# Kernel optimization log

Hardware: AMD Instinct MI355X
Metric: run time of the kernel (lower is better)

Reference implementation:

```python
import jax, jax.numpy as jnp
import numpy as np
import math

N_EMBD = 1024
N_HEAD = 16
BLOCK = 2048
SPARSITY = 0.25
B, T = 2, 2048


def _make_mask_logits(rng):
    # Replicates the patterned init in SparseMixtureAttention.__init__.
    S = BLOCK
    logits = np.empty((N_HEAD, S, S), dtype=np.float32)
    for h in range(N_HEAD):
        if h % 3 == 0:  # banded pattern (bandwidth 16)
            i = np.arange(S)
            band = (np.abs(i[:, None] - i[None, :]) <= 16)
            logits[h] = np.where(band, rng.standard_normal((S, S)) + 2.0,
                                 rng.standard_normal((S, S)) - 2.0)
        elif h % 3 == 1:  # strided pattern: every 4th column
            strided = (np.arange(S)[None, :] % 4 == 0)
            logits[h] = np.where(strided, rng.standard_normal((S, S)) + 2.0,
                                 rng.standard_normal((S, S)) - 2.0)
        else:  # random pattern with given sparsity
            rnd = rng.random((S, S)) < SPARSITY
            logits[h] = np.where(rnd, rng.standard_normal((S, S)) + 2.0,
                                 rng.standard_normal((S, S)) - 2.0)
    # keep the diagonal unmasked so no causal row is fully masked (avoids NaN rows)
    d = np.arange(S)
    logits[:, d, d] = np.abs(logits[:, d, d]) + 2.0
    return logits.astype(np.float32)


def setup_inputs() -> dict:
    key = jax.random.key(0)
    ks = jax.random.split(key, 5)
    rng = np.random.default_rng(0)
    return {
        "x": jax.random.normal(ks[0], (B, T, N_EMBD), dtype=jnp.float32),
        "mask_logits": jnp.asarray(_make_mask_logits(rng)),
        "W_attn": jax.random.normal(ks[1], (3 * N_EMBD, N_EMBD), dtype=jnp.float32) * 0.02,
        "b_attn": jnp.zeros((3 * N_EMBD,), dtype=jnp.float32),
        "W_proj": jax.random.normal(ks[2], (N_EMBD, N_EMBD), dtype=jnp.float32) * 0.02,
        "b_proj": jnp.zeros((N_EMBD,), dtype=jnp.float32),
    }


def reference(x, mask_logits, W_attn, b_attn, W_proj, b_proj):
    Bx, Tx, C = x.shape
    H = mask_logits.shape[0]
    D = C // H
    qkv = x @ W_attn.T + b_attn                       # [B,T,3C]
    q, k, v = jnp.split(qkv, 3, axis=-1)
    q = q.reshape(Bx, Tx, H, D)
    k = k.reshape(Bx, Tx, H, D)
    v = v.reshape(Bx, Tx, H, D)
    att = jnp.einsum('bthd,bshd->bhts', q, k) * (1.0 / math.sqrt(D))  # [B,H,T,T]
    # forward value of the STE mask equals the hard mask (probs - probs.detach() == 0)
    keep = jax.nn.sigmoid(mask_logits[:, :Tx, :Tx]) > 0.5             # [H,T,T]
    causal = jnp.tril(jnp.ones((Tx, Tx), dtype=bool))
    mask = causal[None, :, :] & keep                                  # [H,T,T]
    att = jnp.where(mask[None], att, -jnp.inf)
    att = jax.nn.softmax(att, axis=-1)
    y = jnp.einsum('bhts,bshd->bthd', att, v).reshape(Bx, Tx, C)
    return y @ W_proj.T + b_proj
```

## Files before the change

### kernel.cpp

```cpp
#include <hip/hip_runtime.h>
#include <hip/hip_bf16.h>
#include <stdint.h>

typedef unsigned short u16;
typedef unsigned int u32;
typedef unsigned long long u64;
typedef __attribute__((ext_vector_type(8))) short bf16x8;
typedef __attribute__((ext_vector_type(4))) float f32x4;

#define NB 2
#define NH 16
#define TT 2048
#define DD 64
#define CC 1024

__device__ __forceinline__ u16 bf16bits(float f) {
    __hip_bfloat16 h = __float2bfloat16(f);
    return __builtin_bit_cast(unsigned short, h);
}

__device__ __forceinline__ void gload_lds16(const void* g, void* l) {
    __builtin_amdgcn_global_load_lds(
        (const __attribute__((address_space(1))) void*)g,
        (__attribute__((address_space(3))) void*)l, 16, 0, 0);
}

__global__ __launch_bounds__(256) void prep_all(
    const float* __restrict__ x, const float* __restrict__ Wa_f,
    const float* __restrict__ Wp_f, const float* __restrict__ ml,
    u16* __restrict__ xb, u16* __restrict__ wab, u16* __restrict__ wpb,
    unsigned char* __restrict__ mb) {
    const int bid = blockIdx.x;
    if (bid < 512) {
        int idx = bid * 256 + threadIdx.x;
        for (int i = idx; i < 2097152; i += 512 * 256) {
            const float* src; u16* dst; int off;
            if (i < 1048576)      { src = x;    dst = xb;  off = i; }
            else if (i < 1835008) { src = Wa_f; dst = wab; off = i - 1048576; }
            else                  { src = Wp_f; dst = wpb; off = i - 1835008; }
            float4 v = reinterpret_cast<const float4*>(src)[off];
            ushort4 o;
            o.x = bf16bits(v.x); o.y = bf16bits(v.y);
            o.z = bf16bits(v.z); o.w = bf16bits(v.w);
            reinterpret_cast<ushort4*>(dst)[off] = o;
        }
    } else {
        const int wid = ((bid - 512) << 2) + (threadIdx.x >> 6);
        const int lane = threadIdx.x & 63;
        const int i0 = wid & 2047;
        const int hbase = (wid >> 11) << 3;
#pragma unroll 1
        for (int k = 0; k < 8; ++k) {
            int h = hbase + k;
            int i = (k & 1) ? (2047 - i0) : i0;
            int row = h * 2048 + i;
            const float* src = ml + (size_t)row * TT;
            unsigned char* dst = mb + (size_t)row * (TT / 8);
            for (int c8 = lane; c8 * 8 <= i; c8 += 64) {
                const float4* p = reinterpret_cast<const float4*>(src + c8 * 8);
                float4 a = p[0];
                float4 b = p[1];
                unsigned v = 0;
                v |= (a.x > 0.f) ? 1u : 0u;
                v |= (a.y > 0.f) ? 2u : 0u;
                v |= (a.z > 0.f) ? 4u : 0u;
                v |= (a.w > 0.f) ? 8u : 0u;
                v |= (b.x > 0.f) ? 16u : 0u;
                v |= (b.y > 0.f) ? 32u : 0u;
                v |= (b.z > 0.f) ? 64u : 0u;
                v |= (b.w > 0.f) ? 128u : 0u;
                dst[c8] = (unsigned char)v;
            }
        }
    }
}

template <int MODE>
__global__ __launch_bounds__(256) void gemm_bt(
    const u16* __restrict__ A, const u16* __restrict__ Bw,
    const float* __restrict__ bias,
    u16* __restrict__ Qb, u16* __restrict__ Kb, u16* __restrict__ Vtb,
    float* __restrict__ Cout, int Kdim) {
    const int bm = blockIdx.y * 128;
    const int bn = blockIdx.x * 128;
    const int tid = threadIdx.x;
    const int w = tid >> 6, lane = tid & 63;
    const int lrow = lane & 15, lgrp = lane >> 4;
    const int wr = (w >> 1) * 64, wc = (w & 1) * 64;

    __shared__ __align__(16) u16 ABs[2][128 * 64];
    u16* As = ABs[0];
    u16* Bs = ABs[1];

    f32x4 acc[4][4] = {};

    const int nkt = Kdim >> 6;
    for (int kt = 0; kt < nkt; ++kt) {
        const int k0 = kt << 6;
#pragma unroll
        for (int i = 0; i < 4; ++i) {
            int e = i * 2048 + tid * 8;
            int r = e >> 6, c = e & 63;
            gload_lds16(A + (size_t)(bm + r) * Kdim + k0 + c, (char*)As + i * 4096 + w * 1024);
            gload_lds16(Bw + (size_t)(bn + r) * Kdim + k0 + c, (char*)Bs + i * 4096 + w * 1024);
        }
        __syncthreads();
#pragma unroll
        for (int kk = 0; kk < 2; ++kk) {
            bf16x8 af[4], bfz[4];
#pragma unroll
            for (int i = 0; i < 4; ++i)
                af[i] = *reinterpret_cast<const bf16x8*>(&As[(wr + i * 16 + lrow) * 64 + kk * 32 + lgrp * 8]);
#pragma unroll
            for (int i = 0; i < 4; ++i)
                bfz[i] = *reinterpret_cast<const bf16x8*>(&Bs[(wc + i * 16 + lrow) * 64 + kk * 32 + lgrp * 8]);
#pragma unroll
            for (int mi = 0; mi < 4; ++mi)
#pragma unroll
                for (int ni = 0; ni < 4; ++ni)
                    acc[mi][ni] = __builtin_amdgcn_mfma_f32_16x16x32_bf16(af[mi], bfz[ni], acc[mi][ni], 0, 0, 0);
        }
        __syncthreads();
    }

    const int sec = (MODE == 0) ? (bn >> 10) : 1;

    if (MODE == 0 && sec == 2) {
        u16* Tl = &ABs[0][0];
#pragma unroll
        for (int ni = 0; ni < 4; ++ni) {
            int nl = wc + ni * 16 + lrow;
            float bv = bias[bn + nl];
#pragma unroll
            for (int mi = 0; mi < 4; ++mi) {
                int ml2 = wr + mi * 16 + lgrp * 4;
                u64 pk = 0;
#pragma unroll
                for (int j = 0; j < 4; ++j)
                    pk |= (u64)bf16bits(acc[mi][ni][j] + bv) << (16 * j);
                int byte = nl * 256 + ((ml2 * 2) ^ ((nl & 7) << 4));
                *reinterpret_cast<u64*>((char*)Tl + byte) = pk;
            }
        }
        __syncthreads();
        int r = tid >> 1, half = tid & 1;
        int h = ((bn & 1023) >> 6) + (r >> 6);
        int d = r & 63;
        int b = bm >> 11;
        u16* gdst = Vtb + (((size_t)b * NH + h) * DD + d) * TT + (bm & 2047) + half * 64;
#pragma unroll
        for (int c = 0; c < 8; ++c) {
            uint4 v = *reinterpret_cast<const uint4*>(
                (char*)Tl + r * 256 + ((half * 128 + c * 16) ^ ((r & 7) << 4)));
            *reinterpret_cast<uint4*>(gdst + c * 8) = v;
        }
        return;
    }

#pragma unroll
    for (int ni = 0; ni < 4; ++ni) {
        int n = bn + wc + ni * 16 + lrow;
        float bv = bias[n];
#pragma unroll
        for (int mi = 0; mi < 4; ++mi) {
#pragma unroll
            for (int j = 0; j < 4; ++j) {
                int m = bm + wr + mi * 16 + lgrp * 4 + j;
                float v = acc[mi][ni][j] + bv;
                if (MODE == 1) {
                    Cout[(size_t)m * 1024 + n] = v;
                } else {
                    int h = (n & 1023) >> 6;
                    int d = n & 63;
                    int b = m >> 11;
                    int t = m & 2047;
                    if (sec == 0) {
                        Qb[(((size_t)b * NH + h) * TT + t) * DD + d] =
                            bf16bits(v * (0.125f * 1.4426950408889634f));
                    } else {
                        Kb[(((size_t)b * NH + h) * TT + t) * DD + d] = bf16bits(v);
                    }
                }
            }
        }
    }
}

__global__ __launch_bounds__(256) void attn_kernel(
    const u16* __restrict__ Qb, const u16* __restrict__ Kb,
    const u16* __restrict__ Vtb, const unsigned char* __restrict__ mb,
    u16* __restrict__ att_out) {
    const int slot = blockIdx.x >> 4;
    const int h = blockIdx.x & 15;
    const int b = blockIdx.y;
    const int qt = (slot < 16) ? (31 - slot) : (slot - 16);
    const int tid = threadIdx.x;
    const int w = tid >> 6, lane = tid & 63;
    const int lrow = lane & 15, g = lane >> 4;

    __shared__ __align__(16) u16 Ks[2][64 * 64];
    __shared__ __align__(16) u16 Vts[2][64 * 64];
    __shared__ __align__(16) u16 Ps[4][16 * 64];

    const u16* kg_base = &Kb[((size_t)b * NH + h) * TT * DD];
    const u16* vg_base = &Vtb[((size_t)b * NH + h) * DD * TT];

    auto STAGE = [&](int bufi, int kt) {
#pragma unroll
        for (int i = 0; i < 2; ++i) {
            int e = i * 2048 + tid * 8;
            int r = e >> 6, c = e & 63;
            int cs = c ^ ((r & 7) << 3);
            gload_lds16(kg_base + (size_t)kt * 64 * DD + r * DD + cs,
                        (char*)Ks[bufi] + i * 4096 + w * 1024);
            gload_lds16(vg_base + kt * 64 + (size_t)r * TT + cs,
                        (char*)Vts[bufi] + i * 4096 + w * 1024);
        }
    };

    const int qrow_g = qt * 64 + w * 16 + lrow;
    const int rswz = (lrow & 7) << 4;

    bf16x8 qf[2];
#pragma unroll
    for (int kk = 0; kk < 2; ++kk)
        qf[kk] = *reinterpret_cast<const bf16x8*>(
            &Qb[(((size_t)b * NH + h) * TT + qrow_g) * DD + kk * 32 + g * 8]);

    f32x4 oacc[4] = {};
    float l_run = 0.f;

    const unsigned char* mrow_base = mb + ((size_t)h * TT + qrow_g) * (TT / 8);
    char* PsW = (char*)&Ps[w][0];

    STAGE(0, 0);
    int buf = 0;

#pragma unroll 1
    for (int kt = 0; kt <= qt; ++kt) {
        u64 mw = *reinterpret_cast<const u64*>(mrow_base + kt * 8);
        if (kt < qt) {
            STAGE(buf ^ 1, kt + 1);
            asm volatile("s_waitcnt vmcnt(5)" ::: "memory");
        } else {
            asm volatile("s_waitcnt vmcnt(1)" ::: "memory");
        }
        __builtin_amdgcn_sched_barrier(0);
        asm volatile("s_barrier" ::: "memory");

        f32x4 s[4] = {};
        __builtin_amdgcn_s_setprio(1);
#pragma unroll
        for (int kk = 0; kk < 2; ++kk)
#pragma unroll
            for (int nt = 0; nt < 4; ++nt) {
                bf16x8 kf = *reinterpret_cast<const bf16x8*>(
                    (char*)Ks[buf] + (((nt * 16 + lrow) * 128 + (kk * 32 + g * 8) * 2) ^ rswz));
                s[nt] = __builtin_amdgcn_mfma_f32_16x16x32_bf16(kf, qf[kk], s[nt], 0, 0, 0);
            }
        __builtin_amdgcn_s_setprio(0);

        u64 mws = mw >> (g * 4);
        u32 mlo = (u32)mws, mhi = (u32)(mws >> 32);
        float rs = 0.f;
        if (kt == qt) {
#pragma unroll
            for (int nt = 0; nt < 4; ++nt)
#pragma unroll
                for (int j = 0; j < 4; ++j) {
                    int bi = nt * 16 + j;
                    bool keep = (((bi < 32 ? mlo : mhi) >> (bi & 31)) & 1) &&
                                (kt * 64 + nt * 16 + g * 4 + j <= qrow_g);
                    float p = keep ? exp2f(s[nt][j]) : 0.f;
                    rs += p;
                    s[nt][j] = p;
                }
        } else {
#pragma unroll
            for (int nt = 0; nt < 4; ++nt)
#pragma unroll
                for (int j = 0; j < 4; ++j) {
                    int bi = nt * 16 + j;
                    bool keep = ((bi < 32 ? mlo : mhi) >> (bi & 31)) & 1;
                    float p = keep ? exp2f(s[nt][j]) : 0.f;
                    rs += p;
                    s[nt][j] = p;
                }
        }
        rs += __shfl_xor(rs, 16);
        rs += __shfl_xor(rs, 32);
        l_run += rs;

#pragma unroll
        for (int nt = 0; nt < 4; ++nt)
#pragma unroll
            for (int t = 0; t < 2; ++t) {
                u32 pk = (u32)bf16bits(s[nt][2 * t]) |
                         ((u32)bf16bits(s[nt][2 * t + 1]) << 16);
                int byte = (lrow * 128 + (nt * 16 + g * 4 + 2 * t) * 2) ^ rswz;
                *reinterpret_cast<u32*>(PsW + byte) = pk;
            }

        __builtin_amdgcn_s_setprio(1);
#pragma unroll
        for (int kk = 0; kk < 2; ++kk) {
            bf16x8 pf = *reinterpret_cast<const bf16x8*>(
                PsW + ((lrow * 128 + (kk * 32 + g * 8) * 2) ^ rswz));
#pragma unroll
            for (int dt = 0; dt < 4; ++dt) {
                bf16x8 vf = *reinterpret_cast<const bf16x8*>(
                    (char*)Vts[buf] + (((dt * 16 + lrow) * 128 + (kk * 32 + g * 8) * 2) ^ rswz));
                oacc[dt] = __builtin_amdgcn_mfma_f32_16x16x32_bf16(pf, vf, oacc[dt], 0, 0, 0);
            }
        }
        __builtin_amdgcn_s_setprio(0);

        asm volatile("s_barrier" ::: "memory");
        buf ^= 1;
    }

    float lb[4];
#pragma unroll
    for (int j = 0; j < 4; ++j)
        lb[j] = __shfl(l_run, (lane & 48) + g * 4 + j);
#pragma unroll
    for (int dt = 0; dt < 4; ++dt)
#pragma unroll
        for (int j = 0; j < 4; ++j) {
            int t = qt * 64 + w * 16 + g * 4 + j;
            float o = oacc[dt][j] / lb[j];
            att_out[((size_t)b * TT + t) * CC + h * DD + dt * 16 + lrow] = bf16bits(o);
        }
}

extern "C" void kernel_launch(void* const* d_in, const int* in_sizes, int n_in,
                              void* d_out, int out_size, void* d_ws, size_t ws_size,
                              hipStream_t stream) {
    const float* x = (const float*)d_in[0];
    const float* mask_logits = (const float*)d_in[1];
    const float* W_attn = (const float*)d_in[2];
    const float* b_attn = (const float*)d_in[3];
    const float* W_proj = (const float*)d_in[4];
    const float* b_proj = (const float*)d_in[5];
    float* out = (float*)d_out;

    char* ws = (char*)d_ws;
    u16* xb  = (u16*)(ws + 0);
    u16* Wa  = (u16*)(ws + (8u << 20));
    u16* Wp  = (u16*)(ws + (14u << 20));
    u16* Qb  = (u16*)(ws + (16u << 20));
    u16* Kb  = (u16*)(ws + (24u << 20));
    u16* Vtb = (u16*)(ws + (32u << 20));
    u16* att = (u16*)(ws + (40u << 20));
    unsigned char* mbits = (unsigned char*)(ws + (48u << 20));

    prep_all<<<1536, 256, 0, stream>>>(x, W_attn, W_proj, mask_logits,
                                       xb, Wa, Wp, mbits);
    gemm_bt<0><<<dim3(24, 32), 256, 0, stream>>>(xb, Wa, b_attn, Qb, Kb, Vtb, nullptr, CC);
    attn_kernel<<<dim3(512, 2), 256, 0, stream>>>(Qb, Kb, Vtb, mbits, att);
    gemm_bt<1><<<dim3(8, 32), 256, 0, stream>>>(att, Wp, b_proj, nullptr, nullptr, nullptr, out, CC);
}
```

Before: 165.6 us.

## Process 128 query rows per attention block to share staged K/V tiles

The attention kernel now runs 512-thread blocks with 8 waves covering 128 query rows, so each staged 64-row K/V tile in LDS serves twice as many query rows. The block count halves, and each thread issues one global-to-LDS load per tensor per stage instead of two. Waves whose query rows lie entirely before a key tile skip the compute for that tile but still take part in the barriers. This halves K/V global traffic per query row, at the cost of idle waves on the final diagonal tile and fewer, larger blocks.

After: 166.9 us. About the same (+0.8%).

```diff
diff --git a/kernel.cpp b/kernel.cpp
--- a/kernel.cpp
+++ b/kernel.cpp
@@ -186,39 +186,40 @@
     }
 }
 
-__global__ __launch_bounds__(256) void attn_kernel(
+__global__ __launch_bounds__(512, 4) void attn_kernel(
     const u16* __restrict__ Qb, const u16* __restrict__ Kb,
     const u16* __restrict__ Vtb, const unsigned char* __restrict__ mb,
     u16* __restrict__ att_out) {
-    const int slot = blockIdx.x >> 4;
-    const int h = blockIdx.x & 15;
-    const int b = blockIdx.y;
-    const int qt = (slot < 16) ? (31 - slot) : (slot - 16);
+    const int bid = blockIdx.x;
+    const int s = bid >> 5;
+    const int hb = bid & 31;
+    const int h = hb >> 1, b = hb & 1;
+    const int qc = (s < 8) ? (15 - s) : (s - 8);
+    const int nkt = 2 * qc + 2;
+
     const int tid = threadIdx.x;
-    const int w = tid >> 6, lane = tid & 63;
+    const int wv = tid >> 6, lane = tid & 63;
     const int lrow = lane & 15, g = lane >> 4;
 
     __shared__ __align__(16) u16 Ks[2][64 * 64];
     __shared__ __align__(16) u16 Vts[2][64 * 64];
-    __shared__ __align__(16) u16 Ps[4][16 * 64];
+    __shared__ __align__(16) u16 Ps[8][16 * 64];
 
     const u16* kg_base = &Kb[((size_t)b * NH + h) * TT * DD];
     const u16* vg_base = &Vtb[((size_t)b * NH + h) * DD * TT];
 
     auto STAGE = [&](int bufi, int kt) {
-#pragma unroll
-        for (int i = 0; i < 2; ++i) {
-            int e = i * 2048 + tid * 8;
-            int r = e >> 6, c = e & 63;
-            int cs = c ^ ((r & 7) << 3);
-            gload_lds16(kg_base + (size_t)kt * 64 * DD + r * DD + cs,
-                        (char*)Ks[bufi] + i * 4096 + w * 1024);
-            gload_lds16(vg_base + kt * 64 + (size_t)r * TT + cs,
-                        (char*)Vts[bufi] + i * 4096 + w * 1024);
-        }
+        int r = tid >> 3;
+        int c = (tid & 7) * 8;
+        int cs = c ^ ((r & 7) << 3);
+        gload_lds16(kg_base + (size_t)kt * 64 * DD + r * DD + cs,
+                    (char*)Ks[bufi] + wv * 1024);
+        gload_lds16(vg_base + kt * 64 + (size_t)r * TT + cs,
+                    (char*)Vts[bufi] + wv * 1024);
     };
 
-    const int qrow_g = qt * 64 + w * 16 + lrow;
+    const int qrow_g = qc * 128 + wv * 16 + lrow;
+    const int diag_w = 2 * qc + (wv >> 2);
     const int rswz = (lrow & 7) << 4;
 
     bf16x8 qf[2];
@@ -231,89 +232,91 @@
     float l_run = 0.f;
 
     const unsigned char* mrow_base = mb + ((size_t)h * TT + qrow_g) * (TT / 8);
-    char* PsW = (char*)&Ps[w][0];
+    char* PsW = (char*)&Ps[wv][0];
 
     STAGE(0, 0);
     int buf = 0;
 
 #pragma unroll 1
-    for (int kt = 0; kt <= qt; ++kt) {
+    for (int kt = 0; kt < nkt; ++kt) {
         u64 mw = *reinterpret_cast<const u64*>(mrow_base + kt * 8);
-        if (kt < qt) {
+        if (kt + 1 < nkt) {
             STAGE(buf ^ 1, kt + 1);
-            asm volatile("s_waitcnt vmcnt(5)" ::: "memory");
+            asm volatile("s_waitcnt vmcnt(3)" ::: "memory");
         } else {
             asm volatile("s_waitcnt vmcnt(1)" ::: "memory");
         }
         __builtin_amdgcn_sched_barrier(0);
         asm volatile("s_barrier" ::: "memory");
 
-        f32x4 s[4] = {};
-        __builtin_amdgcn_s_setprio(1);
-#pragma unroll
-        for (int kk = 0; kk < 2; ++kk)
-#pragma unroll
-            for (int nt = 0; nt < 4; ++nt) {
-                bf16x8 kf = *reinterpret_cast<const bf16x8*>(
-                    (char*)Ks[buf] + (((nt * 16 + lrow) * 128 + (kk * 32 + g * 8) * 2) ^ rswz));
-                s[nt] = __builtin_amdgcn_mfma_f32_16x16x32_bf16(kf, qf[kk], s[nt], 0, 0, 0);
-            }
-        __builtin_amdgcn_s_setprio(0);
-
-        u64 mws = mw >> (g * 4);
-        u32 mlo = (u32)mws, mhi = (u32)(mws >> 32);
-        float rs = 0.f;
-        if (kt == qt) {
+        if (kt <= diag_w) {
+            f32x4 sv[4] = {};
+            __builtin_amdgcn_s_setprio(1);
+#pragma unroll
+            for (int kk = 0; kk < 2; ++kk)
+#pragma unroll
+                for (int nt = 0; nt < 4; ++nt) {
+                    bf16x8 kf = *reinterpret_cast<const bf16x8*>(
+                        (char*)Ks[buf] + (((nt * 16 + lrow) * 128 + (kk * 32 + g * 8) * 2) ^ rswz));
+                    sv[nt] = __builtin_amdgcn_mfma_f32_16x16x32_bf16(kf, qf[kk], sv[nt], 0, 0, 0);
+                }
+            __builtin_amdgcn_s_setprio(0);
+
+            u64 mws = mw >> (g * 4);
+            u32 mlo = (u32)mws, mhi = (u32)(mws >> 32);
+            float rs = 0.f;
+            if (kt == diag_w) {
+#pragma unroll
+                for (int nt = 0; nt < 4; ++nt)
+#pragma unroll
+                    for (int j = 0; j < 4; ++j) {
+                        int bi = nt * 16 + j;
+                        bool keep = (((bi < 32 ? mlo : mhi) >> (bi & 31)) & 1) &&
+                                    (kt * 64 + nt * 16 + g * 4 + j <= qrow_g);
+                        float p = keep ? exp2f(sv[nt][j]) : 0.f;
+                        rs += p;
+                        sv[nt][j] = p;
+                    }
+            } else {
+#pragma unroll
+                for (int nt = 0; nt < 4; ++nt)
+#pragma unroll
+                    for (int j = 0; j < 4; ++j) {
+                        int bi = nt * 16 + j;
+                        bool keep = ((bi < 32 ? mlo : mhi) >> (bi & 31)) & 1;
+                        float p = keep ? exp2f(sv[nt][j]) : 0.f;
+                        rs += p;
+                        sv[nt][j] = p;
+                    }
+            }
+            rs += __shfl_xor(rs, 16);
+            rs += __shfl_xor(rs, 32);
+            l_run += rs;
+
 #pragma unroll
             for (int nt = 0; nt < 4; ++nt)
 #pragma unroll
-                for (int j = 0; j < 4; ++j) {
-                    int bi = nt * 16 + j;
-                    bool keep = (((bi < 32 ? mlo : mhi) >> (bi & 31)) & 1) &&
-                                (kt * 64 + nt * 16 + g * 4 + j <= qrow_g);
-                    float p = keep ? exp2f(s[nt][j]) : 0.f;
-                    rs += p;
-                    s[nt][j] = p;
+                for (int t = 0; t < 2; ++t) {
+                    u32 pk = (u32)bf16bits(sv[nt][2 * t]) |
+                             ((u32)bf16bits(sv[nt][2 * t + 1]) << 16);
+                    int byte = (lrow * 128 + (nt * 16 + g * 4 + 2 * t) * 2) ^ rswz;
+                    *reinterpret_cast<u32*>(PsW + byte) = pk;
                 }
-        } else {
-#pragma unroll
-            for (int nt = 0; nt < 4; ++nt)
-#pragma unroll
-                for (int j = 0; j < 4; ++j) {
-                    int bi = nt * 16 + j;
-                    bool keep = ((bi < 32 ? mlo : mhi) >> (bi & 31)) & 1;
-                    float p = keep ? exp2f(s[nt][j]) : 0.f;
-                    rs += p;
-                    s[nt][j] = p;
+
+            __builtin_amdgcn_s_setprio(1);
+#pragma unroll
+            for (int kk = 0; kk < 2; ++kk) {
+                bf16x8 pf = *reinterpret_cast<const bf16x8*>(
+                    PsW + ((lrow * 128 + (kk * 32 + g * 8) * 2) ^ rswz));
+#pragma unroll
+                for (int dt = 0; dt < 4; ++dt) {
+                    bf16x8 vf = *reinterpret_cast<const bf16x8*>(
+                        (char*)Vts[buf] + (((dt * 16 + lrow) * 128 + (kk * 32 + g * 8) * 2) ^ rswz));
+                    oacc[dt] = __builtin_amdgcn_mfma_f32_16x16x32_bf16(pf, vf, oacc[dt], 0, 0, 0);
                 }
-        }
-        rs += __shfl_xor(rs, 16);
-        rs += __shfl_xor(rs, 32);
-        l_run += rs;
-
-#pragma unroll
-        for (int nt = 0; nt < 4; ++nt)
-#pragma unroll
-            for (int t = 0; t < 2; ++t) {
-                u32 pk = (u32)bf16bits(s[nt][2 * t]) |
-                         ((u32)bf16bits(s[nt][2 * t + 1]) << 16);
-                int byte = (lrow * 128 + (nt * 16 + g * 4 + 2 * t) * 2) ^ rswz;
-                *reinterpret_cast<u32*>(PsW + byte) = pk;
-            }
-
-        __builtin_amdgcn_s_setprio(1);
-#pragma unroll
-        for (int kk = 0; kk < 2; ++kk) {
-            bf16x8 pf = *reinterpret_cast<const bf16x8*>(
-                PsW + ((lrow * 128 + (kk * 32 + g * 8) * 2) ^ rswz));
-#pragma unroll
-            for (int dt = 0; dt < 4; ++dt) {
-                bf16x8 vf = *reinterpret_cast<const bf16x8*>(
-                    (char*)Vts[buf] + (((dt * 16 + lrow) * 128 + (kk * 32 + g * 8) * 2) ^ rswz));
-                oacc[dt] = __builtin_amdgcn_mfma_f32_16x16x32_bf16(pf, vf, oacc[dt], 0, 0, 0);
-            }
-        }
-        __builtin_amdgcn_s_setprio(0);
+            }
+            __builtin_amdgcn_s_setprio(0);
+        }
 
         asm volatile("s_barrier" ::: "memory");
         buf ^= 1;
@@ -327,7 +330,7 @@
     for (int dt = 0; dt < 4; ++dt)
 #pragma unroll
         for (int j = 0; j < 4; ++j) {
-            int t = qt * 64 + w * 16 + g * 4 + j;
+            int t = qc * 128 + wv * 16 + g * 4 + j;
             float o = oacc[dt][j] / lb[j];
             att_out[((size_t)b * TT + t) * CC + h * DD + dt * 16 + lrow] = bf16bits(o);
         }
@@ -357,6 +360,6 @@
     prep_all<<<1536, 256, 0, stream>>>(x, W_attn, W_proj, mask_logits,
                                        xb, Wa, Wp, mbits);
     gemm_bt<0><<<dim3(24, 32), 256, 0, stream>>>(xb, Wa, b_attn, Qb, Kb, Vtb, nullptr, CC);
-    attn_kernel<<<dim3(512, 2), 256, 0, stream>>>(Qb, Kb, Vtb, mbits, att);
+    attn_kernel<<<512, 512, 0, stream>>>(Qb, Kb, Vtb, mbits, att);
     gemm_bt<1><<<dim3(8, 32), 256, 0, stream>>>(att, Wp, b_proj, nullptr, nullptr, nullptr, out, CC);
 }
```

## Load K and V fragments directly from global memory instead of LDS staging

Applied to the files above, without the earlier changes.

Removes the double-buffered LDS staging of K and V tiles, along with the per-iteration barriers. Each wave now loads its MFMA operand fragments straight from global memory into registers. This drops LDS traffic and block-wide synchronisation. In exchange, the four waves load the same K/V data redundantly, each global load is a strided 16-byte access, and there is no prefetch overlap across iterations.

Result: slower. 265.4 us (+60.3%).

```diff
diff --git a/kernel.cpp b/kernel.cpp
--- a/kernel.cpp
+++ b/kernel.cpp
@@ -198,25 +198,10 @@
     const int w = tid >> 6, lane = tid & 63;
     const int lrow = lane & 15, g = lane >> 4;
 
-    __shared__ __align__(16) u16 Ks[2][64 * 64];
-    __shared__ __align__(16) u16 Vts[2][64 * 64];
     __shared__ __align__(16) u16 Ps[4][16 * 64];
 
-    const u16* kg_base = &Kb[((size_t)b * NH + h) * TT * DD];
-    const u16* vg_base = &Vtb[((size_t)b * NH + h) * DD * TT];
-
-    auto STAGE = [&](int bufi, int kt) {
-#pragma unroll
-        for (int i = 0; i < 2; ++i) {
-            int e = i * 2048 + tid * 8;
-            int r = e >> 6, c = e & 63;
-            int cs = c ^ ((r & 7) << 3);
-            gload_lds16(kg_base + (size_t)kt * 64 * DD + r * DD + cs,
-                        (char*)Ks[bufi] + i * 4096 + w * 1024);
-            gload_lds16(vg_base + kt * 64 + (size_t)r * TT + cs,
-                        (char*)Vts[bufi] + i * 4096 + w * 1024);
-        }
-    };
+    const u16* kg = &Kb[((size_t)b * NH + h) * TT * DD];
+    const u16* vg = &Vtb[((size_t)b * NH + h) * DD * TT];
 
     const int qrow_g = qt * 64 + w * 16 + lrow;
     const int rswz = (lrow & 7) << 4;
@@ -233,32 +218,37 @@
     const unsigned char* mrow_base = mb + ((size_t)h * TT + qrow_g) * (TT / 8);
     char* PsW = (char*)&Ps[w][0];
 
-    STAGE(0, 0);
-    int buf = 0;
+    const u16* kbase = kg + (size_t)lrow * DD + g * 8;
+    const u16* vbase = vg + (size_t)lrow * TT + g * 8;
 
 #pragma unroll 1
     for (int kt = 0; kt <= qt; ++kt) {
         u64 mw = *reinterpret_cast<const u64*>(mrow_base + kt * 8);
-        if (kt < qt) {
-            STAGE(buf ^ 1, kt + 1);
-            asm volatile("s_waitcnt vmcnt(5)" ::: "memory");
-        } else {
-            asm volatile("s_waitcnt vmcnt(1)" ::: "memory");
-        }
-        __builtin_amdgcn_sched_barrier(0);
-        asm volatile("s_barrier" ::: "memory");
+
+        bf16x8 kf[8];
+#pragma unroll
+        for (int kk = 0; kk < 2; ++kk)
+#pragma unroll
+            for (int nt = 0; nt < 4; ++nt)
+                kf[kk * 4 + nt] = *reinterpret_cast<const bf16x8*>(
+                    kbase + (size_t)(kt * 64 + nt * 16) * DD + kk * 32);
 
         f32x4 s[4] = {};
         __builtin_amdgcn_s_setprio(1);
 #pragma unroll
         for (int kk = 0; kk < 2; ++kk)
 #pragma unroll
-            for (int nt = 0; nt < 4; ++nt) {
-                bf16x8 kf = *reinterpret_cast<const bf16x8*>(
-                    (char*)Ks[buf] + (((nt * 16 + lrow) * 128 + (kk * 32 + g * 8) * 2) ^ rswz));
-                s[nt] = __builtin_amdgcn_mfma_f32_16x16x32_bf16(kf, qf[kk], s[nt], 0, 0, 0);
-            }
+            for (int nt = 0; nt < 4; ++nt)
+                s[nt] = __builtin_amdgcn_mfma_f32_16x16x32_bf16(kf[kk * 4 + nt], qf[kk], s[nt], 0, 0, 0);
         __builtin_amdgcn_s_setprio(0);
+
+        bf16x8 vv[8];
+#pragma unroll
+        for (int kk = 0; kk < 2; ++kk)
+#pragma unroll
+            for (int dt = 0; dt < 4; ++dt)
+                vv[kk * 4 + dt] = *reinterpret_cast<const bf16x8*>(
+                    vbase + (size_t)(dt * 16) * TT + kt * 64 + kk * 32);
 
         u64 mws = mw >> (g * 4);
         u32 mlo = (u32)mws, mhi = (u32)(mws >> 32);
@@ -307,16 +297,10 @@
             bf16x8 pf = *reinterpret_cast<const bf16x8*>(
                 PsW + ((lrow * 128 + (kk * 32 + g * 8) * 2) ^ rswz));
 #pragma unroll
-            for (int dt = 0; dt < 4; ++dt) {
-                bf16x8 vf = *reinterpret_cast<const bf16x8*>(
-                    (char*)Vts[buf] + (((dt * 16 + lrow) * 128 + (kk * 32 + g * 8) * 2) ^ rswz));
-                oacc[dt] = __builtin_amdgcn_mfma_f32_16x16x32_bf16(pf, vf, oacc[dt], 0, 0, 0);
-            }
+            for (int dt = 0; dt < 4; ++dt)
+                oacc[dt] = __builtin_amdgcn_mfma_f32_16x16x32_bf16(pf, vv[kk * 4 + dt], oacc[dt], 0, 0, 0);
         }
         __builtin_amdgcn_s_setprio(0);
-
-        asm volatile("s_barrier" ::: "memory");
-        buf ^= 1;
     }
 
     float lb[4];
```
